# Kernel optimization log

Hardware: AMD Instinct MI355X
Metric: run time of the kernel (lower is better)

Reference implementation:

```python
import jax, jax.numpy as jnp
import numpy as np

B, N_STATES, STATE_SIZE = 32768, 16, 32
ENC, HID, OUT = 64, 128, 8


def setup_inputs() -> dict:
    key = jax.random.key(0)
    ks = jax.random.split(key, 8)
    states = jax.random.normal(ks[0], (B, N_STATES, STATE_SIZE), dtype=jnp.float32)
    # validity flags: first element of each per-field state. agent state (index 0)
    # always valid; neighbor states valid with prob 0.7 (contiguity enforced in reference
    # via cumprod, matching the original while-loop semantics).
    flags = (jax.random.uniform(ks[1], (B, N_STATES)) < 0.7).astype(jnp.float32)
    flags = flags.at[:, 0].set(1.0)
    states = states.at[:, :, 0].set(flags)
    obs_flat = states.reshape(B, N_STATES * STATE_SIZE)
    s = 0.05
    return {
        "obs_flat": obs_flat,
        "W_enc": jax.random.normal(ks[2], (STATE_SIZE, ENC), dtype=jnp.float32) * s,
        "b_enc": jnp.zeros((ENC,), dtype=jnp.float32),
        "W_f": jax.random.normal(ks[3], (2 * ENC, HID), dtype=jnp.float32) * s,
        "b_f": jnp.zeros((HID,), dtype=jnp.float32),
        "W_dec": jax.random.normal(ks[4], (HID, OUT), dtype=jnp.float32) * s,
        "b_dec": jnp.zeros((OUT,), dtype=jnp.float32),
    }


def reference(obs_flat, W_enc, b_enc, W_f, b_f, W_dec, b_dec):
    Bsz = obs_flat.shape[0]
    states = obs_flat.reshape(Bsz, N_STATES, STATE_SIZE)          # [B,N,S]
    flags = states[:, :, 0]                                        # [B,N]
    # original: while-loop stops at first invalid state -> contiguous-prefix validity
    neigh_valid = jnp.cumprod((flags[:, 1:] == 1.0).astype(jnp.float32), axis=1)  # [B,N-1]
    enc = jax.nn.relu(jnp.einsum('bns,se->bne', states, W_enc) + b_enc)            # [B,N,E]
    agent_enc = enc[:, 0]                                          # [B,E]
    neigh_enc = enc[:, 1:]                                         # [B,N-1,E]
    cnt = jnp.sum(neigh_valid, axis=1)                             # [B]
    # mean aggregation over valid neighbors; zero vector if none (original aggregates [zeros])
    agg = jnp.einsum('bne,bn->be', neigh_enc, neigh_valid) / jnp.maximum(cnt, 1.0)[:, None]
    f_in = jnp.concatenate([agent_enc, agg], axis=-1)              # [B,2E]
    hidden = jax.nn.relu(f_in @ W_f + b_f)                         # [B,H]
    logits = hidden @ W_dec + b_dec                                # [B,O]
    return logits
```

## Files before the change

kernel.cpp:

```cpp
#include <hip/hip_runtime.h>
#include <stdint.h>

#define NB    32768
#define NS    16
#define SS    32
#define ENCD  64
#define HIDD  128
#define OUTD  8
#define BT    16
#define THREADS 256

typedef _Float16 half8  __attribute__((ext_vector_type(8)));
typedef __fp16   fp16x2 __attribute__((ext_vector_type(2)));
typedef float    f32x4  __attribute__((ext_vector_type(4)));

#define MFMA(a, b, c) __builtin_amdgcn_mfma_f32_16x16x32_f16((a), (b), (c), 0, 0, 0)

__device__ __forceinline__ void split8(const float* f, half8& hi, half8& lo) {
#pragma unroll
  for (int j = 0; j < 8; j += 2) {
    fp16x2 h  = __builtin_amdgcn_cvt_pkrtz(f[j], f[j + 1]);
    float  r0 = f[j]     - (float)h[0];
    float  r1 = f[j + 1] - (float)h[1];
    fp16x2 l2 = __builtin_amdgcn_cvt_pkrtz(r0, r1);
    hi[j] = (_Float16)(float)h[0];  hi[j + 1] = (_Float16)(float)h[1];
    lo[j] = (_Float16)(float)l2[0]; lo[j + 1] = (_Float16)(float)l2[1];
  }
}

__global__ __launch_bounds__(THREADS, 6)
void gnn_fused(const float* __restrict__ obs,
               const float* __restrict__ W_enc,
               const float* __restrict__ b_enc,
               const float* __restrict__ W_f,
               const float* __restrict__ b_f,
               const float* __restrict__ W_dec,
               const float* __restrict__ b_dec,
               float* __restrict__ out)
{
  __shared__ __align__(16) float f_in[BT][132];
  __shared__ __align__(16) float hidn[BT][132];

  const int tid  = threadIdx.x;
  const int w    = tid >> 6;
  const int l    = tid & 63;
  const int m15  = l & 15;
  const int quad = l >> 4;
  const int b0   = blockIdx.x * BT;

  half8 we_hi[4], we_lo[4];
  float benc[4];
#pragma unroll
  for (int nt = 0; nt < 4; ++nt) {
    float f[8];
#pragma unroll
    for (int j = 0; j < 8; ++j)
      f[j] = W_enc[(size_t)(quad * 8 + j) * ENCD + nt * 16 + m15];
    split8(f, we_hi[nt], we_lo[nt]);
    benc[nt] = b_enc[nt * 16 + m15];
  }

  const float* bp = obs + (size_t)(b0 + w * 4) * (NS * SS) + m15 * SS + quad * 8;
  float4 c0 = ((const float4*)bp)[0];
  float4 c1 = ((const float4*)bp)[1];
#pragma unroll
  for (int i = 0; i < 4; ++i) {
    float4 n0, n1;
    if (i < 3) {
      const float* np = bp + (size_t)(i + 1) * (NS * SS);
      n0 = ((const float4*)np)[0];
      n1 = ((const float4*)np)[1];
    } else { n0 = c0; n1 = c1; }

    float f[8] = {c0.x, c0.y, c0.z, c0.w, c1.x, c1.y, c1.z, c1.w};

    unsigned long long bal = __ballot((l < 16) && (f[0] == 1.0f));
    int run = __builtin_ctzll(~(bal >> 1));
    float inv = 1.0f / fmaxf((float)run, 1.0f);

    half8 ahi, alo;
    split8(f, ahi, alo);

    const int bi = w * 4 + i;
#pragma unroll
    for (int nt = 0; nt < 4; ++nt) {
      f32x4 acc = {0.f, 0.f, 0.f, 0.f};
      acc = MFMA(ahi, we_hi[nt], acc);
      acc = MFMA(alo, we_hi[nt], acc);
      acc = MFMA(ahi, we_lo[nt], acc);
      float s = 0.f, e0 = 0.f;
#pragma unroll
      for (int r = 0; r < 4; ++r) {
        int n = quad * 4 + r;
        float v = fmaxf(acc[r] + benc[nt], 0.f);
        if (n == 0) e0 = v;
        if (n >= 1 && n <= run) s += v;
      }
      s += __shfl_xor(s, 16, 64);
      s += __shfl_xor(s, 32, 64);
      if (quad == 0) {
        f_in[bi][nt * 16 + m15]      = e0;
        f_in[bi][64 + nt * 16 + m15] = s * inv;
      }
    }
    c0 = n0; c1 = n1;
  }
  __syncthreads();

  {
    half8 fa_hi[4], fa_lo[4];
#pragma unroll
    for (int ks = 0; ks < 4; ++ks) {
      const float4* p = (const float4*)&f_in[m15][ks * 32 + quad * 8];
      float4 a = p[0], b = p[1];
      float f[8] = {a.x, a.y, a.z, a.w, b.x, b.y, b.z, b.w};
      split8(f, fa_hi[ks], fa_lo[ks]);
    }

#pragma unroll
    for (int tt = 0; tt < 2; ++tt) {
      const int h0 = (w * 2 + tt) * 16 + m15;
      f32x4 acc = {0.f, 0.f, 0.f, 0.f};
#pragma unroll
      for (int ks = 0; ks < 4; ++ks) {
        float f[8];
#pragma unroll
        for (int j = 0; j < 8; ++j)
          f[j] = W_f[(size_t)(ks * 32 + quad * 8 + j) * HIDD + h0];
        half8 bhi, blo;
        split8(f, bhi, blo);
        acc = MFMA(fa_hi[ks], bhi, acc);
        acc = MFMA(fa_lo[ks], bhi, acc);
        acc = MFMA(fa_hi[ks], blo, acc);
      }
      const float bfv = b_f[h0];
#pragma unroll
      for (int r = 0; r < 4; ++r)
        hidn[quad * 4 + r][h0] = fmaxf(acc[r] + bfv, 0.f);
    }
  }
  __syncthreads();

  if (w == 0) {
    half8 ga_hi[4], ga_lo[4];
#pragma unroll
    for (int ks = 0; ks < 4; ++ks) {
      const float4* p = (const float4*)&hidn[m15][ks * 32 + quad * 8];
      float4 a = p[0], b = p[1];
      float f[8] = {a.x, a.y, a.z, a.w, b.x, b.y, b.z, b.w};
      split8(f, ga_hi[ks], ga_lo[ks]);
    }
    f32x4 acc = {0.f, 0.f, 0.f, 0.f};
#pragma unroll
    for (int ks = 0; ks < 4; ++ks) {
      float f[8];
#pragma unroll
      for (int j = 0; j < 8; ++j) {
        int k = ks * 32 + quad * 8 + j;
        f[j] = (m15 < OUTD) ? W_dec[(size_t)k * OUTD + m15] : 0.f;
      }
      half8 bhi, blo;
      split8(f, bhi, blo);
      acc = MFMA(ga_hi[ks], bhi, acc);
      acc = MFMA(ga_lo[ks], bhi, acc);
      acc = MFMA(ga_hi[ks], blo, acc);
    }
    if (m15 < OUTD) {
      const float bd = b_dec[m15];
#pragma unroll
      for (int r = 0; r < 4; ++r) {
        const int m = quad * 4 + r;
        out[(size_t)(b0 + m) * OUTD + m15] = acc[r] + bd;
      }
    }
  }
}

extern "C" void kernel_launch(void* const* d_in, const int* in_sizes, int n_in,
                              void* d_out, int out_size, void* d_ws, size_t ws_size,
                              hipStream_t stream) {
  (void)in_sizes; (void)n_in; (void)d_ws; (void)ws_size; (void)out_size;
  const float* obs   = (const float*)d_in[0];
  const float* W_enc = (const float*)d_in[1];
  const float* b_enc = (const float*)d_in[2];
  const float* W_f   = (const float*)d_in[3];
  const float* b_f   = (const float*)d_in[4];
  const float* W_dec = (const float*)d_in[5];
  const float* b_dec = (const float*)d_in[6];
  float* out = (float*)d_out;

  dim3 grid(NB / BT);
  dim3 block(THREADS);
  gnn_fused<<<grid, block, 0, stream>>>(obs, W_enc, b_enc, W_f, b_f, W_dec, b_dec, out);
}
```

Before: 111.3 us.

## Precompute split fp16 weight fragments in prep kernel and deepen obs prefetch

Adds a small prep kernel that converts W_enc, W_f and W_dec into hi/lo fp16 MFMA fragment layout in workspace once per call. The main kernel then loads ready fragments with coalesced 16-byte loads instead of strided scalar loads plus per-block split conversion. The obs load pipeline is also changed to prefetch two batch rows ahead rather than one. This adds an extra kernel launch and workspace traffic, and depends on the workspace being large enough.

```diff
diff --git a/kernel.cpp b/kernel.cpp
--- a/kernel.cpp
+++ b/kernel.cpp
@@ -10,6 +10,13 @@
 #define BT    16
 #define THREADS 256
 
+#define WE_FRAGS 8
+#define WF_FRAGS 64
+#define WD_FRAGS 8
+#define WE_OFF 0
+#define WF_OFF (WE_FRAGS)
+#define WD_OFF (WE_FRAGS + WF_FRAGS)
+
 typedef _Float16 half8  __attribute__((ext_vector_type(8)));
 typedef __fp16   fp16x2 __attribute__((ext_vector_type(2)));
 typedef float    f32x4  __attribute__((ext_vector_type(4)));
@@ -28,19 +35,55 @@
   }
 }
 
+__global__ void prep_weights(const float* __restrict__ We,
+                             const float* __restrict__ Wf,
+                             const float* __restrict__ Wd,
+                             _Float16* __restrict__ ws) {
+  const int g = blockIdx.x * 256 + threadIdx.x;
+  half8* frag = (half8*)ws;
+  float f[8];
+  half8 hi, lo;
+  if (g < 256) {
+    const int nt = g >> 6, l = g & 63, quad = l >> 4, m15 = l & 15;
+#pragma unroll
+    for (int j = 0; j < 8; ++j)
+      f[j] = We[(size_t)(quad * 8 + j) * ENCD + nt * 16 + m15];
+    split8(f, hi, lo);
+    frag[(WE_OFF + nt * 2 + 0) * 64 + l] = hi;
+    frag[(WE_OFF + nt * 2 + 1) * 64 + l] = lo;
+  } else if (g < 256 + 2048) {
+    const int e = g - 256;
+    const int nt = e >> 8, ks = (e >> 6) & 3, l = e & 63, quad = l >> 4, m15 = l & 15;
+#pragma unroll
+    for (int j = 0; j < 8; ++j)
+      f[j] = Wf[(size_t)(ks * 32 + quad * 8 + j) * HIDD + nt * 16 + m15];
+    split8(f, hi, lo);
+    frag[(WF_OFF + (nt * 4 + ks) * 2 + 0) * 64 + l] = hi;
+    frag[(WF_OFF + (nt * 4 + ks) * 2 + 1) * 64 + l] = lo;
+  } else {
+    const int e = g - 2304;
+    const int ks = e >> 6, l = e & 63, quad = l >> 4, m15 = l & 15;
+#pragma unroll
+    for (int j = 0; j < 8; ++j)
+      f[j] = (m15 < OUTD) ? Wd[(size_t)(ks * 32 + quad * 8 + j) * OUTD + m15] : 0.f;
+    split8(f, hi, lo);
+    frag[(WD_OFF + ks * 2 + 0) * 64 + l] = hi;
+    frag[(WD_OFF + ks * 2 + 1) * 64 + l] = lo;
+  }
+}
+
 __global__ __launch_bounds__(THREADS, 6)
 void gnn_fused(const float* __restrict__ obs,
-               const float* __restrict__ W_enc,
                const float* __restrict__ b_enc,
-               const float* __restrict__ W_f,
                const float* __restrict__ b_f,
-               const float* __restrict__ W_dec,
                const float* __restrict__ b_dec,
+               const _Float16* __restrict__ wsf,
                float* __restrict__ out)
 {
   __shared__ __align__(16) float f_in[BT][132];
   __shared__ __align__(16) float hidn[BT][132];
 
+  const half8* frag = (const half8*)wsf;
   const int tid  = threadIdx.x;
   const int w    = tid >> 6;
   const int l    = tid & 63;
@@ -52,27 +95,28 @@
   float benc[4];
 #pragma unroll
   for (int nt = 0; nt < 4; ++nt) {
-    float f[8];
-#pragma unroll
-    for (int j = 0; j < 8; ++j)
-      f[j] = W_enc[(size_t)(quad * 8 + j) * ENCD + nt * 16 + m15];
-    split8(f, we_hi[nt], we_lo[nt]);
-    benc[nt] = b_enc[nt * 16 + m15];
+    we_hi[nt] = frag[(WE_OFF + nt * 2 + 0) * 64 + l];
+    we_lo[nt] = frag[(WE_OFF + nt * 2 + 1) * 64 + l];
+    benc[nt]  = b_enc[nt * 16 + m15];
   }
 
   const float* bp = obs + (size_t)(b0 + w * 4) * (NS * SS) + m15 * SS + quad * 8;
-  float4 c0 = ((const float4*)bp)[0];
-  float4 c1 = ((const float4*)bp)[1];
+  float4 cc0[4], cc1[4];
+#pragma unroll
+  for (int i = 0; i < 2; ++i) {
+    const float* p = bp + (size_t)i * (NS * SS);
+    cc0[i] = ((const float4*)p)[0];
+    cc1[i] = ((const float4*)p)[1];
+  }
 #pragma unroll
   for (int i = 0; i < 4; ++i) {
-    float4 n0, n1;
-    if (i < 3) {
-      const float* np = bp + (size_t)(i + 1) * (NS * SS);
-      n0 = ((const float4*)np)[0];
-      n1 = ((const float4*)np)[1];
-    } else { n0 = c0; n1 = c1; }
-
-    float f[8] = {c0.x, c0.y, c0.z, c0.w, c1.x, c1.y, c1.z, c1.w};
+    if (i < 2) {
+      const float* p = bp + (size_t)(i + 2) * (NS * SS);
+      cc0[i + 2] = ((const float4*)p)[0];
+      cc1[i + 2] = ((const float4*)p)[1];
+    }
+    float f[8] = {cc0[i].x, cc0[i].y, cc0[i].z, cc0[i].w,
+                  cc1[i].x, cc1[i].y, cc1[i].z, cc1[i].w};
 
     unsigned long long bal = __ballot((l < 16) && (f[0] == 1.0f));
     int run = __builtin_ctzll(~(bal >> 1));
@@ -103,7 +147,6 @@
         f_in[bi][64 + nt * 16 + m15] = s * inv;
       }
     }
-    c0 = n0; c1 = n1;
   }
   __syncthreads();
 
@@ -119,16 +162,13 @@
 
 #pragma unroll
     for (int tt = 0; tt < 2; ++tt) {
-      const int h0 = (w * 2 + tt) * 16 + m15;
+      const int ntile = w * 2 + tt;
+      const int h0 = ntile * 16 + m15;
       f32x4 acc = {0.f, 0.f, 0.f, 0.f};
 #pragma unroll
       for (int ks = 0; ks < 4; ++ks) {
-        float f[8];
-#pragma unroll
-        for (int j = 0; j < 8; ++j)
-          f[j] = W_f[(size_t)(ks * 32 + quad * 8 + j) * HIDD + h0];
-        half8 bhi, blo;
-        split8(f, bhi, blo);
+        half8 bhi = frag[(WF_OFF + (ntile * 4 + ks) * 2 + 0) * 64 + l];
+        half8 blo = frag[(WF_OFF + (ntile * 4 + ks) * 2 + 1) * 64 + l];
         acc = MFMA(fa_hi[ks], bhi, acc);
         acc = MFMA(fa_lo[ks], bhi, acc);
         acc = MFMA(fa_hi[ks], blo, acc);
@@ -153,14 +193,8 @@
     f32x4 acc = {0.f, 0.f, 0.f, 0.f};
 #pragma unroll
     for (int ks = 0; ks < 4; ++ks) {
-      float f[8];
-#pragma unroll
-      for (int j = 0; j < 8; ++j) {
-        int k = ks * 32 + quad * 8 + j;
-        f[j] = (m15 < OUTD) ? W_dec[(size_t)k * OUTD + m15] : 0.f;
-      }
-      half8 bhi, blo;
-      split8(f, bhi, blo);
+      half8 bhi = frag[(WD_OFF + ks * 2 + 0) * 64 + l];
+      half8 blo = frag[(WD_OFF + ks * 2 + 1) * 64 + l];
       acc = MFMA(ga_hi[ks], bhi, acc);
       acc = MFMA(ga_lo[ks], bhi, acc);
       acc = MFMA(ga_hi[ks], blo, acc);
@@ -179,7 +213,7 @@
 extern "C" void kernel_launch(void* const* d_in, const int* in_sizes, int n_in,
                               void* d_out, int out_size, void* d_ws, size_t ws_size,
                               hipStream_t stream) {
-  (void)in_sizes; (void)n_in; (void)d_ws; (void)ws_size; (void)out_size;
+  (void)in_sizes; (void)n_in; (void)ws_size; (void)out_size;
   const float* obs   = (const float*)d_in[0];
   const float* W_enc = (const float*)d_in[1];
   const float* b_enc = (const float*)d_in[2];
@@ -188,8 +222,9 @@
   const float* W_dec = (const float*)d_in[5];
   const float* b_dec = (const float*)d_in[6];
   float* out = (float*)d_out;
-
-  dim3 grid(NB / BT);
-  dim3 block(THREADS);
-  gnn_fused<<<grid, block, 0, stream>>>(obs, W_enc, b_enc, W_f, b_f, W_dec, b_dec, out);
-}
+  _Float16* wsf = (_Float16*)d_ws;
+
+  prep_weights<<<dim3(10), dim3(256), 0, stream>>>(W_enc, W_f, W_dec, wsf);
+  gnn_fused<<<dim3(NB / BT), dim3(THREADS), 0, stream>>>(
+      obs, b_enc, b_f, b_dec, (const _Float16*)wsf, out);
+}
```

Measured after the change: 124.0 us. 11.4% more time.

## Replace split-fp16 emulated fp32 MFMAs with single fp16 MFMAs and fp16 LDS

Applied to the files above, without the earlier changes.

Drops the hi/lo fp16 splitting that emulated fp32 precision with three MFMAs per tile and uses one fp16 MFMA per tile in all three layers. Intermediate activations in shared memory are stored as fp16, halving LDS traffic and removing the per-element split conversion. All four obs row loads are now issued up front instead of being software-pipelined one ahead. This trades accuracy against the fp32 reference for fewer instructions and registers.

```diff
diff --git a/kernel.cpp b/kernel.cpp
--- a/kernel.cpp
+++ b/kernel.cpp
@@ -10,22 +10,16 @@
 #define BT    16
 #define THREADS 256
 
-typedef _Float16 half8  __attribute__((ext_vector_type(8)));
-typedef __fp16   fp16x2 __attribute__((ext_vector_type(2)));
-typedef float    f32x4  __attribute__((ext_vector_type(4)));
+typedef _Float16 half8 __attribute__((ext_vector_type(8)));
+typedef float    f32x4 __attribute__((ext_vector_type(4)));
 
 #define MFMA(a, b, c) __builtin_amdgcn_mfma_f32_16x16x32_f16((a), (b), (c), 0, 0, 0)
 
-__device__ __forceinline__ void split8(const float* f, half8& hi, half8& lo) {
+__device__ __forceinline__ half8 pack8(const float* f) {
+  half8 h;
 #pragma unroll
-  for (int j = 0; j < 8; j += 2) {
-    fp16x2 h  = __builtin_amdgcn_cvt_pkrtz(f[j], f[j + 1]);
-    float  r0 = f[j]     - (float)h[0];
-    float  r1 = f[j + 1] - (float)h[1];
-    fp16x2 l2 = __builtin_amdgcn_cvt_pkrtz(r0, r1);
-    hi[j] = (_Float16)(float)h[0];  hi[j + 1] = (_Float16)(float)h[1];
-    lo[j] = (_Float16)(float)l2[0]; lo[j + 1] = (_Float16)(float)l2[1];
-  }
+  for (int j = 0; j < 8; ++j) h[j] = (_Float16)f[j];
+  return h;
 }
 
 __global__ __launch_bounds__(THREADS, 6)
@@ -38,8 +32,8 @@
                const float* __restrict__ b_dec,
                float* __restrict__ out)
 {
-  __shared__ __align__(16) float f_in[BT][132];
-  __shared__ __align__(16) float hidn[BT][132];
+  __shared__ __align__(16) _Float16 f_in[BT][136];
+  __shared__ __align__(16) _Float16 hidn[BT][136];
 
   const int tid  = threadIdx.x;
   const int w    = tid >> 6;
@@ -48,7 +42,7 @@
   const int quad = l >> 4;
   const int b0   = blockIdx.x * BT;
 
-  half8 we_hi[4], we_lo[4];
+  half8 we[4];
   float benc[4];
 #pragma unroll
   for (int nt = 0; nt < 4; ++nt) {
@@ -56,38 +50,34 @@
 #pragma unroll
     for (int j = 0; j < 8; ++j)
       f[j] = W_enc[(size_t)(quad * 8 + j) * ENCD + nt * 16 + m15];
-    split8(f, we_hi[nt], we_lo[nt]);
+    we[nt]   = pack8(f);
     benc[nt] = b_enc[nt * 16 + m15];
   }
 
   const float* bp = obs + (size_t)(b0 + w * 4) * (NS * SS) + m15 * SS + quad * 8;
-  float4 c0 = ((const float4*)bp)[0];
-  float4 c1 = ((const float4*)bp)[1];
+  float4 c0[4], c1[4];
 #pragma unroll
   for (int i = 0; i < 4; ++i) {
-    float4 n0, n1;
-    if (i < 3) {
-      const float* np = bp + (size_t)(i + 1) * (NS * SS);
-      n0 = ((const float4*)np)[0];
-      n1 = ((const float4*)np)[1];
-    } else { n0 = c0; n1 = c1; }
-
-    float f[8] = {c0.x, c0.y, c0.z, c0.w, c1.x, c1.y, c1.z, c1.w};
+    const float* p = bp + (size_t)i * (NS * SS);
+    c0[i] = ((const float4*)p)[0];
+    c1[i] = ((const float4*)p)[1];
+  }
+#pragma unroll
+  for (int i = 0; i < 4; ++i) {
+    float f[8] = {c0[i].x, c0[i].y, c0[i].z, c0[i].w,
+                  c1[i].x, c1[i].y, c1[i].z, c1[i].w};
 
     unsigned long long bal = __ballot((l < 16) && (f[0] == 1.0f));
     int run = __builtin_ctzll(~(bal >> 1));
     float inv = 1.0f / fmaxf((float)run, 1.0f);
 
-    half8 ahi, alo;
-    split8(f, ahi, alo);
+    half8 a = pack8(f);
 
     const int bi = w * 4 + i;
 #pragma unroll
     for (int nt = 0; nt < 4; ++nt) {
       f32x4 acc = {0.f, 0.f, 0.f, 0.f};
-      acc = MFMA(ahi, we_hi[nt], acc);
-      acc = MFMA(alo, we_hi[nt], acc);
-      acc = MFMA(ahi, we_lo[nt], acc);
+      acc = MFMA(a, we[nt], acc);
       float s = 0.f, e0 = 0.f;
 #pragma unroll
       for (int r = 0; r < 4; ++r) {
@@ -99,23 +89,18 @@
       s += __shfl_xor(s, 16, 64);
       s += __shfl_xor(s, 32, 64);
       if (quad == 0) {
-        f_in[bi][nt * 16 + m15]      = e0;
-        f_in[bi][64 + nt * 16 + m15] = s * inv;
+        f_in[bi][nt * 16 + m15]      = (_Float16)e0;
+        f_in[bi][64 + nt * 16 + m15] = (_Float16)(s * inv);
       }
     }
-    c0 = n0; c1 = n1;
   }
   __syncthreads();
 
   {
-    half8 fa_hi[4], fa_lo[4];
+    half8 fa[4];
 #pragma unroll
-    for (int ks = 0; ks < 4; ++ks) {
-      const float4* p = (const float4*)&f_in[m15][ks * 32 + quad * 8];
-      float4 a = p[0], b = p[1];
-      float f[8] = {a.x, a.y, a.z, a.w, b.x, b.y, b.z, b.w};
-      split8(f, fa_hi[ks], fa_lo[ks]);
-    }
+    for (int ks = 0; ks < 4; ++ks)
+      fa[ks] = *(const half8*)&f_in[m15][ks * 32 + quad * 8];
 
 #pragma unroll
     for (int tt = 0; tt < 2; ++tt) {
@@ -127,29 +112,21 @@
 #pragma unroll
         for (int j = 0; j < 8; ++j)
           f[j] = W_f[(size_t)(ks * 32 + quad * 8 + j) * HIDD + h0];
-        half8 bhi, blo;
-        split8(f, bhi, blo);
-        acc = MFMA(fa_hi[ks], bhi, acc);
-        acc = MFMA(fa_lo[ks], bhi, acc);
-        acc = MFMA(fa_hi[ks], blo, acc);
+        acc = MFMA(fa[ks], pack8(f), acc);
       }
       const float bfv = b_f[h0];
 #pragma unroll
       for (int r = 0; r < 4; ++r)
-        hidn[quad * 4 + r][h0] = fmaxf(acc[r] + bfv, 0.f);
+        hidn[quad * 4 + r][h0] = (_Float16)fmaxf(acc[r] + bfv, 0.f);
     }
   }
   __syncthreads();
 
   if (w == 0) {
-    half8 ga_hi[4], ga_lo[4];
+    half8 ga[4];
 #pragma unroll
-    for (int ks = 0; ks < 4; ++ks) {
-      const float4* p = (const float4*)&hidn[m15][ks * 32 + quad * 8];
-      float4 a = p[0], b = p[1];
-      float f[8] = {a.x, a.y, a.z, a.w, b.x, b.y, b.z, b.w};
-      split8(f, ga_hi[ks], ga_lo[ks]);
-    }
+    for (int ks = 0; ks < 4; ++ks)
+      ga[ks] = *(const half8*)&hidn[m15][ks * 32 + quad * 8];
     f32x4 acc = {0.f, 0.f, 0.f, 0.f};
 #pragma unroll
     for (int ks = 0; ks < 4; ++ks) {
@@ -159,11 +136,7 @@
         int k = ks * 32 + quad * 8 + j;
         f[j] = (m15 < OUTD) ? W_dec[(size_t)k * OUTD + m15] : 0.f;
       }
-      half8 bhi, blo;
-      split8(f, bhi, blo);
-      acc = MFMA(ga_hi[ks], bhi, acc);
-      acc = MFMA(ga_lo[ks], bhi, acc);
-      acc = MFMA(ga_hi[ks], blo, acc);
+      acc = MFMA(ga[ks], pack8(f), acc);
     }
     if (m15 < OUTD) {
       const float bd = b_dec[m15];
@@ -189,7 +162,6 @@
   const float* b_dec = (const float*)d_in[6];
   float* out = (float*)d_out;
 
-  dim3 grid(NB / BT);
-  dim3 block(THREADS);
-  gnn_fused<<<grid, block, 0, stream>>>(obs, W_enc, b_enc, W_f, b_f, W_dec, b_dec, out);
+  gnn_fused<<<dim3(NB / BT), dim3(THREADS), 0, stream>>>(
+      obs, W_enc, b_enc, W_f, b_f, W_dec, b_dec, out);
 }
```

Measured after the change: 114.1 us. 2.5% more time.
